# Kernel tuning notes

Measured on AMD Instinct MI355X. Metric: run time of the kernel, lower is better.

The kernel has to match this reference:

```python
import jax, jax.numpy as jnp
import numpy as np

B, L, E = 256, 4096, 64   # batch, seq_len, d_token
D = 128                   # d_model
H, DH = 4, 16             # attn heads, head dim
SH = 256                  # synapse_hidden
M = 8                     # memory_len
NED = 16                  # neuron_embed_dim
NH = 64                   # nlm_hidden
T = 8                     # n_ticks


def setup_inputs() -> dict:
    key = jax.random.key(0)
    ks = jax.random.split(key, 24)
    rn = lambda k, shape, fan: jax.random.normal(k, shape, jnp.float32) / np.sqrt(fan)
    return {
        "tokens": jax.random.normal(ks[0], (B, L, E), jnp.float32),
        "z0": jnp.zeros((D,), jnp.float32),
        "a0": jnp.zeros((D, M), jnp.float32),
        "ln_g": jnp.ones((D,), jnp.float32),
        "ln_b": jnp.zeros((D,), jnp.float32),
        "Wq": rn(ks[1], (E, D), D), "bq": jnp.zeros((E,), jnp.float32),
        "Wiq": rn(ks[2], (E, E), E), "biq": jnp.zeros((E,), jnp.float32),
        "Wik": rn(ks[3], (E, E), E), "bik": jnp.zeros((E,), jnp.float32),
        "Wiv": rn(ks[4], (E, E), E), "biv": jnp.zeros((E,), jnp.float32),
        "Wo": rn(ks[5], (E, E), E), "bo": jnp.zeros((E,), jnp.float32),
        "Ws1": rn(ks[6], (2 * SH, D + E), D + E), "bs1": jnp.zeros((2 * SH,), jnp.float32),
        "Ws2": rn(ks[7], (D, SH), SH), "bs2": jnp.zeros((D,), jnp.float32),
        "Wn1": rn(ks[8], (NH, M + NED), M + NED), "bn1": jnp.zeros((NH,), jnp.float32),
        "Wn2": rn(ks[9], (1, NH), NH), "bn2": jnp.zeros((1,), jnp.float32),
        "emb": jax.random.normal(ks[10], (D, NED), jnp.float32),
    }


def reference(tokens, z0, a0, ln_g, ln_b, Wq, bq, Wiq, biq, Wik, bik, Wiv, biv,
              Wo, bo, Ws1, bs1, Ws2, bs2, Wn1, bn1, Wn2, bn2, emb):
    b = tokens.shape[0]
    # K/V projections are tick-invariant -> compute once. (B,L,H,DH)
    k = (tokens @ Wik.T + bik).reshape(b, L, H, DH)
    v = (tokens @ Wiv.T + biv).reshape(b, L, H, DH)
    scale = 1.0 / np.sqrt(DH)

    def tick(carry, _):
        z, ah = carry  # z: (B,D), ah: (B,D,M)
        # query head: LayerNorm + Linear(D->E)
        mu = jnp.mean(z, -1, keepdims=True)
        var = jnp.mean((z - mu) ** 2, -1, keepdims=True)
        zn = (z - mu) * jax.lax.rsqrt(var + 1e-5) * ln_g + ln_b
        q = zn @ Wq.T + bq                               # (B,E)
        qh = (q @ Wiq.T + biq).reshape(b, H, DH)         # (B,H,DH)
        # single-query cross-attention
        scores = jnp.einsum("bhd,blhd->bhl", qh, k) * scale
        attw = jax.nn.softmax(scores, axis=-1)
        o = jnp.einsum("bhl,blhd->bhd", attw, v).reshape(b, E)
        o = o @ Wo.T + bo                                # (B,E)
        # synapse GLU-MLP
        s = jnp.concatenate([z, o], axis=-1) @ Ws1.T + bs1
        g1, g2 = jnp.split(s, 2, axis=-1)
        a = (g1 * jax.nn.sigmoid(g2)) @ Ws2.T + bs2      # (B,D)
        # roll history
        ah = jnp.concatenate([ah[:, :, 1:], a[:, :, None]], axis=-1)
        # per-neuron shared NLM with neuron embedding
        inp = jnp.concatenate([ah, jnp.broadcast_to(emb, (b, D, NED))], axis=-1)
        h = jax.nn.silu(inp @ Wn1.T + bn1)               # (B,D,NH)
        z_next = (h @ Wn2.T + bn2)[..., 0]               # (B,D)
        z = jnp.tanh(z_next)
        return (z, ah), z

    z = jnp.broadcast_to(z0, (b, D))
    ah = jnp.broadcast_to(a0, (b, D, M))
    _, zs = jax.lax.scan(tick, (z, ah), None, length=T)  # (T,B,D)
    return jnp.transpose(zs, (1, 0, 2))                  # (B,T,D)
```

## Files before the change

### kernel.cpp

```cpp
#include <hip/hip_runtime.h>

#define B_   256
#define L_   4096
#define E_   64
#define D_   128
#define H_   4
#define DH_  16
#define SH_  256
#define M_   8
#define NED_ 16
#define NH_  64
#define T_   8

typedef __attribute__((ext_vector_type(8))) short short8;
typedef __attribute__((ext_vector_type(4))) float f32x4;
typedef __attribute__((ext_vector_type(4))) unsigned int uint4v;
typedef __attribute__((ext_vector_type(2))) unsigned int uint2v;

#if defined(__has_builtin)
#if __has_builtin(__builtin_amdgcn_sdot4)
#define HAS_SDOT 1
#endif
#endif
#ifndef HAS_SDOT
#define HAS_SDOT 0
#endif

__device__ __forceinline__ float bf2f(unsigned short u) {
  union { unsigned int i; float f; } v; v.i = ((unsigned int)u) << 16; return v.f;
}
__device__ __forceinline__ unsigned short f2bf(float f) {
  union { float f; unsigned int i; } v; v.f = f;
  unsigned int x = v.i;
  return (unsigned short)((x + 0x7fffu + ((x >> 16) & 1u)) >> 16);
}
__device__ __forceinline__ float bflo(unsigned int u){ union { unsigned int i; float f; } v; v.i = u << 16;          return v.f; }
__device__ __forceinline__ float bfhi(unsigned int u){ union { unsigned int i; float f; } v; v.i = u & 0xffff0000u;  return v.f; }
__device__ __forceinline__ unsigned int pk2(float a, float b){
  return (unsigned int)f2bf(a) | ((unsigned int)f2bf(b) << 16);
}
__device__ __forceinline__ unsigned int pk4i(f32x4 x, float r) {
  const int a0 = (int)rintf(x[0] * r);
  const int a1 = (int)rintf(x[1] * r);
  const int a2 = (int)rintf(x[2] * r);
  const int a3 = (int)rintf(x[3] * r);
  return (unsigned int)(a0 & 255) | ((unsigned int)(a1 & 255) << 8) |
         ((unsigned int)(a2 & 255) << 16) | ((unsigned int)(a3 & 255) << 24);
}

template<int MODE>
__device__ __forceinline__ bool mode_ok(const void* ln_g) {
  const unsigned int w = ((const unsigned int*)ln_g)[0];
  return (w == 0x3F800000u) ? (MODE == 0) : (MODE == 1);
}
template<int MODE>
__device__ __forceinline__ float ldw(const void* p, long i) {
  if (MODE) return bf2f(((const unsigned short*)p)[i]);
  return ((const float*)p)[i];
}
template<int MODE>
__device__ __forceinline__ void stw(void* p, long i, float v) {
  if (MODE) ((unsigned short*)p)[i] = f2bf(v);
  else      ((float*)p)[i] = v;
}
template<int MODE>
__device__ __forceinline__ f32x4 ld4(const void* p, long off) {
  f32x4 r;
  if (MODE) {
    const uint2v u = *(const uint2v*)((const unsigned short*)p + off);
    r[0] = bflo(u[0]); r[1] = bfhi(u[0]); r[2] = bflo(u[1]); r[3] = bfhi(u[1]);
  } else {
    r = *(const f32x4*)((const float*)p + off);
  }
  return r;
}
template<int MODE>
__device__ __forceinline__ short8 ld8(const void* p, long off) {
  short8 r;
  if (MODE) {
    r = *(const short8*)((const unsigned short*)p + off);
  } else {
    const float* f = (const float*)p + off;
    const f32x4 f0 = *(const f32x4*)f;
    const f32x4 f1 = *(const f32x4*)(f + 4);
#pragma unroll
    for (int i = 0; i < 4; ++i) {
      r[i]     = (short)f2bf(f0[i]);
      r[4 + i] = (short)f2bf(f1[i]);
    }
  }
  return r;
}

template<int MODE>
__global__ void prep_kernel(const void* __restrict__ ln_g,
                            const void* __restrict__ Wik, const void* __restrict__ Wiv,
                            const void* __restrict__ Ws1, const void* __restrict__ Ws2,
                            unsigned short* __restrict__ Wbf,
                            float* __restrict__ Ws1T, float* __restrict__ Ws2T)
{
  if (!mode_ok<MODE>(ln_g)) return;
  const int idx = blockIdx.x * 256 + threadIdx.x;
  if (idx < 8192) {
    const float v = (idx < 4096) ? ldw<MODE>(Wik, idx) : ldw<MODE>(Wiv, idx - 4096);
    Wbf[idx] = f2bf(v);
  } else if (idx < 8192 + 98304) {
    const int j = idx - 8192;
    const int i = j >> 9, u = j & 511;
    Ws1T[j] = ldw<MODE>(Ws1, (long)u * 192 + i);
  } else if (idx < 8192 + 98304 + 32768) {
    const int j = idx - 8192 - 98304;
    const int i = j >> 7, u = j & 127;
    Ws2T[j] = ldw<MODE>(Ws2, (long)u * 256 + i);
  }
}

template<int MODE>
__global__ __launch_bounds__(256) void kv_proj_kernel(
    const void* __restrict__ ln_g,
    const void* __restrict__ tokens,
    const void* __restrict__ bik, const void* __restrict__ biv,
    const unsigned short* __restrict__ Wbf,
    unsigned char* __restrict__ K8, unsigned char* __restrict__ V8,
    unsigned int* __restrict__ SCb)
{
  if (!mode_ok<MODE>(ln_g)) return;
  const int lane = threadIdx.x & 63;
  const int wv   = threadIdx.x >> 6;
  const int m = lane & 15, quad = lane >> 4;
  const long row0 = (long)blockIdx.x * 128 + wv * 32;

  short8 tb[2][2];
#pragma unroll
  for (int nt = 0; nt < 2; ++nt) {
    const long ar = (row0 + nt * 16 + m) * 64;
    tb[nt][0] = ld8<MODE>(tokens, ar + quad * 8);
    tb[nt][1] = ld8<MODE>(tokens, ar + 32 + quad * 8);
  }

  f32x4 acc[8][2];
#pragma unroll
  for (int mt = 0; mt < 8; ++mt) { acc[mt][0] = 0.f; acc[mt][1] = 0.f; }

#pragma unroll
  for (int kt = 0; kt < 2; ++kt) {
    short8 wa[8];
#pragma unroll
    for (int mt = 0; mt < 8; ++mt)
      wa[mt] = *(const short8*)(Wbf + (mt * 16 + m) * 64 + kt * 32 + quad * 8);
#pragma unroll
    for (int mt = 0; mt < 8; ++mt) {
      acc[mt][0] = __builtin_amdgcn_mfma_f32_16x16x32_bf16(wa[mt], tb[0][kt], acc[mt][0], 0, 0, 0);
      acc[mt][1] = __builtin_amdgcn_mfma_f32_16x16x32_bf16(wa[mt], tb[1][kt], acc[mt][1], 0, 0, 0);
    }
  }

  const long b  = row0 >> 12;
  const int  l0 = (int)(row0 & 4095);
#pragma unroll
  for (int h = 0; h < 4; ++h) {
    const f32x4 bk = ld4<MODE>(bik, h * 16 + quad * 4);
    const f32x4 bv = ld4<MODE>(biv, h * 16 + quad * 4);
    const long rowbase = (b * H_ + h) * (long)L_ + l0;
#pragma unroll
    for (int nt = 0; nt < 2; ++nt) {
      const f32x4 xk = acc[h][nt] + bk;
      const f32x4 xv = acc[h + 4][nt] + bv;
      float ak = fmaxf(fmaxf(fabsf(xk[0]), fabsf(xk[1])), fmaxf(fabsf(xk[2]), fabsf(xk[3])));
      float av = fmaxf(fmaxf(fabsf(xv[0]), fabsf(xv[1])), fmaxf(fabsf(xv[2]), fabsf(xv[3])));
      ak = fmaxf(ak, __shfl_xor(ak, 16)); ak = fmaxf(ak, __shfl_xor(ak, 32));
      av = fmaxf(av, __shfl_xor(av, 16)); av = fmaxf(av, __shfl_xor(av, 32));
      const float rk = ak > 0.f ? 127.f / ak : 0.f;
      const float rv = av > 0.f ? 127.f / av : 0.f;
      const unsigned int uk = pk4i(xk, rk);
      const unsigned int uv = pk4i(xv, rv);
      const long row = rowbase + nt * 16 + m;
      ((unsigned int*)(K8 + row * 16))[quad] = uk;
      ((unsigned int*)(V8 + row * 16))[quad] = uv;
      if (quad == 0)
        SCb[row] = pk2(ak * (1.f / 127.f), av * (1.f / 127.f));
    }
  }
}

template<int MODE>
__global__ __launch_bounds__(1024, 4) void mega_kernel(
    const unsigned char* __restrict__ K8, const unsigned char* __restrict__ V8,
    const unsigned int* __restrict__ SCb,
    const float* __restrict__ Ws1T, const float* __restrict__ Ws2T,
    const void* __restrict__ z0, const void* __restrict__ a0,
    const void* __restrict__ ln_g, const void* __restrict__ ln_b,
    const void* __restrict__ Wq,  const void* __restrict__ bq,
    const void* __restrict__ Wiq, const void* __restrict__ biq,
    const void* __restrict__ Wo,  const void* __restrict__ bo,
    const void* __restrict__ bs1, const void* __restrict__ bs2,
    const void* __restrict__ Wn1, const void* __restrict__ bn1,
    const void* __restrict__ Wn2, const void* __restrict__ bn2,
    const void* __restrict__ emb,
    void* __restrict__ out)
{
  if (!mode_ok<MODE>(ln_g)) return;
  const int b = blockIdx.x, tid = threadIdx.x;
  const int lane = tid & 63, w = tid >> 6;

  __shared__ __align__(16) float z_l[128];
  __shared__ __align__(16) float ah_l[128][8];
  __shared__ __align__(16) float qh_l[64];
  __shared__ __align__(16) unsigned int qi_l[4][4];
  __shared__ float qsc_l[4];
  __shared__ __align__(16) float zo_l[192];
  __shared__ __align__(16) float s_l[512];
  __shared__ __align__(16) float spart[2][512];
  __shared__ __align__(16) float glu_l[256];
  __shared__ __align__(16) float al_l[128];
  __shared__ __align__(16) float p8[8][128];
  __shared__ float part[16][17];
  __shared__ __align__(16) float oat[64];
  __shared__ __align__(16) float znl[128];
  __shared__ __align__(16) float ql[64];
  __shared__ float red[16];

  if (tid < 128) {
    z_l[tid] = ldw<MODE>(z0, tid);
#pragma unroll
    for (int mm = 0; mm < 8; ++mm) ah_l[tid][mm] = ldw<MODE>(a0, tid * 8 + mm);
  }
  __syncthreads();

  for (int phase = 0; phase <= T_; ++phase) {
    if (phase > 0) {
      const int t = phase - 1;
      const int h = tid >> 8, r = tid & 255;
      const unsigned char* kp = K8 + ((long)(b * H_ + h) * L_) * 16;
      const unsigned char* vp = V8 + ((long)(b * H_ + h) * L_) * 16;
      const unsigned int*  scp = SCb + (long)(b * H_ + h) * L_;
#if HAS_SDOT
      const int qi0 = (int)qi_l[h][0], qi1 = (int)qi_l[h][1];
      const int qi2 = (int)qi_l[h][2], qi3 = (int)qi_l[h][3];
      const float qsch = qsc_l[h];
#else
      float q[16];
#pragma unroll
      for (int j = 0; j < 16; ++j) q[j] = qh_l[h * 16 + j] * 0.25f;
#endif
      float ssum = 0.f;
      float o[16];
#pragma unroll
      for (int j = 0; j < 16; ++j) o[j] = 0.f;

#pragma unroll 4
      for (int it = 0; it < 16; ++it) {
        const int l = r + it * 256;
        const uint4v kk = *(const uint4v*)(kp + (long)l * 16);
        const uint4v vv = *(const uint4v*)(vp + (long)l * 16);
        const unsigned int s = scp[l];
#if HAS_SDOT
        int id = 0;
        id = __builtin_amdgcn_sdot4((int)kk[0], qi0, id, false);
        id = __builtin_amdgcn_sdot4((int)kk[1], qi1, id, false);
        id = __builtin_amdgcn_sdot4((int)kk[2], qi2, id, false);
        id = __builtin_amdgcn_sdot4((int)kk[3], qi3, id, false);
        const float sc = (float)id * bflo(s) * qsch;
#else
        float scf = 0.f;
#pragma unroll
        for (int d = 0; d < 4; ++d) {
          const unsigned int u = kk[d];
          scf = fmaf(q[d * 4 + 0], (float)((int)(u << 24) >> 24), scf);
          scf = fmaf(q[d * 4 + 1], (float)((int)(u << 16) >> 24), scf);
          scf = fmaf(q[d * 4 + 2], (float)((int)(u <<  8) >> 24), scf);
          scf = fmaf(q[d * 4 + 3], (float)((int)u >> 24),          scf);
        }
        const float sc = scf * bflo(s);
#endif
        const float pw = __expf(sc);
        ssum += pw;
        const float pv = pw * bfhi(s);
#pragma unroll
        for (int d = 0; d < 4; ++d) {
          const unsigned int u = vv[d];
          o[d * 4 + 0] = fmaf(pv, (float)((int)(u << 24) >> 24), o[d * 4 + 0]);
          o[d * 4 + 1] = fmaf(pv, (float)((int)(u << 16) >> 24), o[d * 4 + 1]);
          o[d * 4 + 2] = fmaf(pv, (float)((int)(u <<  8) >> 24), o[d * 4 + 2]);
          o[d * 4 + 3] = fmaf(pv, (float)((int)u >> 24),          o[d * 4 + 3]);
        }
      }
#pragma unroll
      for (int off = 1; off < 64; off <<= 1) {
        ssum += __shfl_xor(ssum, off);
#pragma unroll
        for (int j = 0; j < 16; ++j) o[j] += __shfl_xor(o[j], off);
      }
      if (lane == 0) {
        part[w][16] = ssum;
#pragma unroll
        for (int j = 0; j < 16; ++j) part[w][j] = o[j];
      }
      __syncthreads();
      if (tid < 128) zo_l[tid] = z_l[tid];
      if (tid < 64) {
        const int hh = tid >> 4, j = tid & 15;
        const float O = part[hh * 4][j] + part[hh * 4 + 1][j] +
                        part[hh * 4 + 2][j] + part[hh * 4 + 3][j];
        const float S = part[hh * 4][16] + part[hh * 4 + 1][16] +
                        part[hh * 4 + 2][16] + part[hh * 4 + 3][16];
        oat[tid] = O / S;
      }
      __syncthreads();
      if (tid < 64) {
        f32x4 av = 0.f;
        const long wr = (long)tid * 64;
#pragma unroll
        for (int i = 0; i < 16; ++i)
          av += (*(const f32x4*)&oat[i * 4]) * ld4<MODE>(Wo, wr + i * 4);
        zo_l[128 + tid] = av[0] + av[1] + av[2] + av[3] + ldw<MODE>(bo, tid);
      }
      __syncthreads();
      {
        const int u = tid & 511, p = tid >> 9;
        float a = 0.f;
#pragma unroll 8
        for (int i = 0; i < 96; ++i)
          a = fmaf(zo_l[p * 96 + i], Ws1T[(p * 96 + i) * 512 + u], a);
        spart[p][u] = a;
      }
      __syncthreads();
      if (tid < 512) s_l[tid] = spart[0][tid] + spart[1][tid] + ldw<MODE>(bs1, tid);
      __syncthreads();
      if (tid < 256)
        glu_l[tid] = s_l[tid] * (1.f / (1.f + __expf(-s_l[tid + 256])));
      __syncthreads();
      {
        const int u = tid & 127, p = tid >> 7;
        float a = 0.f;
#pragma unroll 8
        for (int i = 0; i < 32; ++i)
          a = fmaf(glu_l[p * 32 + i], Ws2T[(p * 32 + i) * 128 + u], a);
        p8[p][u] = a;
      }
      __syncthreads();
      if (tid < 128) {
        float a = ldw<MODE>(bs2, tid);
#pragma unroll
        for (int k = 0; k < 8; ++k) a += p8[k][tid];
        al_l[tid] = a;
      }
      __syncthreads();
      {
        const int d = tid >> 3, p = tid & 7;
        float ahv[8];
#pragma unroll
        for (int c = 0; c < 7; ++c) ahv[c] = ah_l[d][c + 1];
        ahv[7] = al_l[d];
        f32x4 ev[4];
#pragma unroll
        for (int c = 0; c < 4; ++c) ev[c] = ld4<MODE>(emb, d * 16 + c * 4);
        float pr = 0.f;
#pragma unroll
        for (int uu = 0; uu < 8; ++uu) {
          const int u = p * 8 + uu;
          const long wr = (long)u * 24;
          f32x4 av = ld4<MODE>(Wn1, wr) * (*(const f32x4*)&ahv[0])
                   + ld4<MODE>(Wn1, wr + 4) * (*(const f32x4*)&ahv[4]);
#pragma unroll
          for (int c = 0; c < 4; ++c) av += ev[c] * ld4<MODE>(Wn1, wr + 8 + c * 4);
          const float acc = av[0] + av[1] + av[2] + av[3] + ldw<MODE>(bn1, u);
          const float hs = acc * (1.f / (1.f + __expf(-acc)));
          pr = fmaf(hs, ldw<MODE>(Wn2, u), pr);
        }
        pr += __shfl_xor(pr, 1);
        pr += __shfl_xor(pr, 2);
        pr += __shfl_xor(pr, 4);
        const float znew = tanhf(pr + ldw<MODE>(bn2, 0));
        __syncthreads();
        if (p == 0) {
#pragma unroll
          for (int c = 0; c < 8; ++c) ah_l[d][c] = ahv[c];
          z_l[d] = znew;
          stw<MODE>(out, ((long)b * T_ + t) * D_ + d, znew);
        }
      }
      __syncthreads();
      if (t == T_ - 1) break;
    }
    if (tid < 128) {
      const float x = z_l[tid];
      float sx = x, sxx = x * x;
#pragma unroll
      for (int off = 1; off < 64; off <<= 1) {
        sx  += __shfl_xor(sx, off);
        sxx += __shfl_xor(sxx, off);
      }
      if (lane == 0) { red[w] = sx; red[8 + w] = sxx; }
    }
    __syncthreads();
    {
      const float mu  = (red[0] + red[1]) * (1.f / 128.f);
      const float ex2 = (red[8] + red[9]) * (1.f / 128.f);
      const float rstd = rsqrtf(ex2 - mu * mu + 1e-5f);
      if (tid < 128)
        znl[tid] = (z_l[tid] - mu) * rstd * ldw<MODE>(ln_g, tid) + ldw<MODE>(ln_b, tid);
    }
    __syncthreads();
    if (tid < 64) {
      f32x4 av = 0.f;
      const long wr = (long)tid * 128;
#pragma unroll
      for (int i = 0; i < 32; ++i)
        av += (*(const f32x4*)&znl[i * 4]) * ld4<MODE>(Wq, wr + i * 4);
      ql[tid] = av[0] + av[1] + av[2] + av[3] + ldw<MODE>(bq, tid);
    }
    __syncthreads();
    if (tid < 64) {
      f32x4 av = 0.f;
      const long wr = (long)tid * 64;
#pragma unroll
      for (int i = 0; i < 16; ++i)
        av += (*(const f32x4*)&ql[i * 4]) * ld4<MODE>(Wiq, wr + i * 4);
      qh_l[tid] = av[0] + av[1] + av[2] + av[3] + ldw<MODE>(biq, tid);
    }
    __syncthreads();
    if (tid < 4) {
      float am = 0.f;
#pragma unroll
      for (int j = 0; j < 16; ++j) am = fmaxf(am, fabsf(qh_l[tid * 16 + j]));
      const float rq = am > 0.f ? 127.f / am : 0.f;
      qsc_l[tid] = am * (0.25f / 127.f);
#pragma unroll
      for (int dd = 0; dd < 4; ++dd) {
        const int a0 = (int)rintf(qh_l[tid * 16 + dd * 4 + 0] * rq);
        const int a1 = (int)rintf(qh_l[tid * 16 + dd * 4 + 1] * rq);
        const int a2 = (int)rintf(qh_l[tid * 16 + dd * 4 + 2] * rq);
        const int a3 = (int)rintf(qh_l[tid * 16 + dd * 4 + 3] * rq);
        qi_l[tid][dd] = (unsigned int)(a0 & 255) | ((unsigned int)(a1 & 255) << 8) |
                        ((unsigned int)(a2 & 255) << 16) | ((unsigned int)(a3 & 255) << 24);
      }
    }
    __syncthreads();
  }
}

extern "C" void kernel_launch(void* const* d_in, const int* in_sizes, int n_in,
                              void* d_out, int out_size, void* d_ws, size_t ws_size,
                              hipStream_t stream)
{
  const void* tokens = d_in[0];
  const void* z0   = d_in[1];
  const void* a0   = d_in[2];
  const void* ln_g = d_in[3];
  const void* ln_b = d_in[4];
  const void* Wq   = d_in[5];
  const void* bq   = d_in[6];
  const void* Wiq  = d_in[7];
  const void* biq  = d_in[8];
  const void* Wik  = d_in[9];
  const void* bik  = d_in[10];
  const void* Wiv  = d_in[11];
  const void* biv  = d_in[12];
  const void* Wo   = d_in[13];
  const void* bo   = d_in[14];
  const void* Ws1  = d_in[15];
  const void* bs1  = d_in[16];
  const void* Ws2  = d_in[17];
  const void* bs2  = d_in[18];
  const void* Wn1  = d_in[19];
  const void* bn1  = d_in[20];
  const void* Wn2  = d_in[21];
  const void* bn2  = d_in[22];
  const void* emb  = d_in[23];

  const long K8_B = (long)B_ * H_ * L_ * 16;
  const long SC_B = (long)B_ * H_ * L_ * 4;
  char* ws = (char*)d_ws;
  const long offW = 2 * K8_B + SC_B;
  if (ws_size < (size_t)(offW + 16384 + 393216 + 131072)) return;
  unsigned char* K8  = (unsigned char*)(ws);
  unsigned char* V8  = (unsigned char*)(ws + K8_B);
  unsigned int*  SCb = (unsigned int*)(ws + 2 * K8_B);
  unsigned short* Wbf = (unsigned short*)(ws + offW);
  float* Ws1T = (float*)(ws + offW + 16384);
  float* Ws2T = (float*)(ws + offW + 16384 + 393216);

  prep_kernel<0><<<544, 256, 0, stream>>>(ln_g, Wik, Wiv, Ws1, Ws2, Wbf, Ws1T, Ws2T);
  prep_kernel<1><<<544, 256, 0, stream>>>(ln_g, Wik, Wiv, Ws1, Ws2, Wbf, Ws1T, Ws2T);

  kv_proj_kernel<0><<<(B_ * L_) / 128, 256, 0, stream>>>(ln_g, tokens, bik, biv, Wbf, K8, V8, SCb);
  kv_proj_kernel<1><<<(B_ * L_) / 128, 256, 0, stream>>>(ln_g, tokens, bik, biv, Wbf, K8, V8, SCb);

  mega_kernel<0><<<B_, 1024, 0, stream>>>(K8, V8, SCb, Ws1T, Ws2T, z0, a0, ln_g, ln_b,
      Wq, bq, Wiq, biq, Wo, bo, bs1, bs2, Wn1, bn1, Wn2, bn2, emb, d_out);
  mega_kernel<1><<<B_, 1024, 0, stream>>>(K8, V8, SCb, Ws1T, Ws2T, z0, a0, ln_g, ln_b,
      Wq, bq, Wiq, biq, Wo, bo, bs1, bs2, Wn1, bn1, Wn2, bn2, emb, d_out);
}
```

Before: 956.3 us.

## Stage K/V int8 rows into LDS via async global_load_lds with 4-deep pipeline

The attention inner loop now loads K, V and scale rows with global_load_lds into a per-wave 4-slot LDS ring, prefetching three iterations ahead and gating each consume on explicit vmcnt waits. V is stored as offset-binary uint8 so it can be decoded with cheap zero-extends, and the +128 bias is removed at the end with a single fma against the accumulated weight sum. The separate reduction buffers are merged into one scratch array so the large staging buffer fits in LDS. The intent is to hide global-load latency and cut decode ALU work, at the cost of about 147KB of LDS per block, which limits occupancy, plus fragile hand-written waitcnt accounting.

```diff
diff --git a/kernel.cpp b/kernel.cpp
--- a/kernel.cpp
+++ b/kernel.cpp
@@ -12,6 +12,9 @@
 #define NH_  64
 #define T_   8
 
+#define AS1 __attribute__((address_space(1)))
+#define AS3 __attribute__((address_space(3)))
+
 typedef __attribute__((ext_vector_type(8))) short short8;
 typedef __attribute__((ext_vector_type(4))) float f32x4;
 typedef __attribute__((ext_vector_type(4))) unsigned int uint4v;
@@ -44,6 +47,14 @@
   const int a1 = (int)rintf(x[1] * r);
   const int a2 = (int)rintf(x[2] * r);
   const int a3 = (int)rintf(x[3] * r);
+  return (unsigned int)(a0 & 255) | ((unsigned int)(a1 & 255) << 8) |
+         ((unsigned int)(a2 & 255) << 16) | ((unsigned int)(a3 & 255) << 24);
+}
+__device__ __forceinline__ unsigned int pk4u(f32x4 x, float r) {
+  const int a0 = (int)rintf(x[0] * r) + 128;
+  const int a1 = (int)rintf(x[1] * r) + 128;
+  const int a2 = (int)rintf(x[2] * r) + 128;
+  const int a3 = (int)rintf(x[3] * r) + 128;
   return (unsigned int)(a0 & 255) | ((unsigned int)(a1 & 255) << 8) |
          ((unsigned int)(a2 & 255) << 16) | ((unsigned int)(a3 & 255) << 24);
 }
@@ -173,7 +184,7 @@
       const float rk = ak > 0.f ? 127.f / ak : 0.f;
       const float rv = av > 0.f ? 127.f / av : 0.f;
       const unsigned int uk = pk4i(xk, rk);
-      const unsigned int uv = pk4i(xv, rv);
+      const unsigned int uv = pk4u(xv, rv);
       const long row = rowbase + nt * 16 + m;
       ((unsigned int*)(K8 + row * 16))[quad] = uk;
       ((unsigned int*)(V8 + row * 16))[quad] = uv;
@@ -203,6 +214,8 @@
   const int b = blockIdx.x, tid = threadIdx.x;
   const int lane = tid & 63, w = tid >> 6;
 
+  __shared__ __align__(16) char stageb[16 * 4 * 2304];
+  __shared__ __align__(16) float scratch[1024];
   __shared__ __align__(16) float z_l[128];
   __shared__ __align__(16) float ah_l[128][8];
   __shared__ __align__(16) float qh_l[64];
@@ -210,11 +223,8 @@
   __shared__ float qsc_l[4];
   __shared__ __align__(16) float zo_l[192];
   __shared__ __align__(16) float s_l[512];
-  __shared__ __align__(16) float spart[2][512];
   __shared__ __align__(16) float glu_l[256];
   __shared__ __align__(16) float al_l[128];
-  __shared__ __align__(16) float p8[8][128];
-  __shared__ float part[16][17];
   __shared__ __align__(16) float oat[64];
   __shared__ __align__(16) float znl[128];
   __shared__ __align__(16) float ql[64];
@@ -227,13 +237,30 @@
   }
   __syncthreads();
 
+  const int h = w >> 2;
+  const long headrow = ((long)(b * H_) + h) * L_;
+  const char* kp8 = (const char*)K8 + headrow * 16;
+  const char* vp8 = (const char*)V8 + headrow * 16;
+  const char* sp8 = (const char*)SCb + headrow * 4;
+  AS3 char* stg_w = (AS3 char*)stageb + w * (4 * 2304);
+
+#define STAGE(IT) do {                                                          \
+    const long ro_ = (long)((w & 3) * 64) + (long)(IT) * 256;                   \
+    AS3 char* dst_ = stg_w + ((IT) & 3) * 2304;                                 \
+    __builtin_amdgcn_global_load_lds(                                           \
+        (const AS1 unsigned int*)(kp8 + ro_ * 16 + lane * 16),                  \
+        (AS3 unsigned int*)(dst_), 16, 0, 0);                                   \
+    __builtin_amdgcn_global_load_lds(                                           \
+        (const AS1 unsigned int*)(vp8 + ro_ * 16 + lane * 16),                  \
+        (AS3 unsigned int*)(dst_ + 1024), 16, 0, 0);                            \
+    __builtin_amdgcn_global_load_lds(                                           \
+        (const AS1 unsigned int*)(sp8 + ro_ * 4 + lane * 4),                    \
+        (AS3 unsigned int*)(dst_ + 2048), 4, 0, 0);                             \
+  } while (0)
+
   for (int phase = 0; phase <= T_; ++phase) {
     if (phase > 0) {
       const int t = phase - 1;
-      const int h = tid >> 8, r = tid & 255;
-      const unsigned char* kp = K8 + ((long)(b * H_ + h) * L_) * 16;
-      const unsigned char* vp = V8 + ((long)(b * H_ + h) * L_) * 16;
-      const unsigned int*  scp = SCb + (long)(b * H_ + h) * L_;
 #if HAS_SDOT
       const int qi0 = (int)qi_l[h][0], qi1 = (int)qi_l[h][1];
       const int qi2 = (int)qi_l[h][2], qi3 = (int)qi_l[h][3];
@@ -243,48 +270,67 @@
 #pragma unroll
       for (int j = 0; j < 16; ++j) q[j] = qh_l[h * 16 + j] * 0.25f;
 #endif
-      float ssum = 0.f;
+      float ssum = 0.f, spv = 0.f;
       float o[16];
 #pragma unroll
       for (int j = 0; j < 16; ++j) o[j] = 0.f;
 
-#pragma unroll 4
-      for (int it = 0; it < 16; ++it) {
-        const int l = r + it * 256;
-        const uint4v kk = *(const uint4v*)(kp + (long)l * 16);
-        const uint4v vv = *(const uint4v*)(vp + (long)l * 16);
-        const unsigned int s = scp[l];
+      STAGE(0); STAGE(1); STAGE(2);
+
 #if HAS_SDOT
-        int id = 0;
-        id = __builtin_amdgcn_sdot4((int)kk[0], qi0, id, false);
-        id = __builtin_amdgcn_sdot4((int)kk[1], qi1, id, false);
-        id = __builtin_amdgcn_sdot4((int)kk[2], qi2, id, false);
-        id = __builtin_amdgcn_sdot4((int)kk[3], qi3, id, false);
+#define SCORE(kk)                                                              \
+        int id = 0;                                                            \
+        id = __builtin_amdgcn_sdot4((int)kk[0], qi0, id, false);               \
+        id = __builtin_amdgcn_sdot4((int)kk[1], qi1, id, false);               \
+        id = __builtin_amdgcn_sdot4((int)kk[2], qi2, id, false);               \
+        id = __builtin_amdgcn_sdot4((int)kk[3], qi3, id, false);               \
         const float sc = (float)id * bflo(s) * qsch;
 #else
-        float scf = 0.f;
-#pragma unroll
-        for (int d = 0; d < 4; ++d) {
-          const unsigned int u = kk[d];
-          scf = fmaf(q[d * 4 + 0], (float)((int)(u << 24) >> 24), scf);
-          scf = fmaf(q[d * 4 + 1], (float)((int)(u << 16) >> 24), scf);
-          scf = fmaf(q[d * 4 + 2], (float)((int)(u <<  8) >> 24), scf);
-          scf = fmaf(q[d * 4 + 3], (float)((int)u >> 24),          scf);
-        }
+#define SCORE(kk)                                                              \
+        float scf = 0.f;                                                       \
+        _Pragma("unroll")                                                      \
+        for (int d_ = 0; d_ < 4; ++d_) {                                       \
+          const unsigned int u_ = kk[d_];                                      \
+          scf = fmaf(q[d_ * 4 + 0], (float)((int)(u_ << 24) >> 24), scf);      \
+          scf = fmaf(q[d_ * 4 + 1], (float)((int)(u_ << 16) >> 24), scf);      \
+          scf = fmaf(q[d_ * 4 + 2], (float)((int)(u_ <<  8) >> 24), scf);      \
+          scf = fmaf(q[d_ * 4 + 3], (float)((int)u_ >> 24),          scf);     \
+        }                                                                      \
         const float sc = scf * bflo(s);
 #endif
-        const float pw = __expf(sc);
-        ssum += pw;
-        const float pv = pw * bfhi(s);
-#pragma unroll
-        for (int d = 0; d < 4; ++d) {
-          const unsigned int u = vv[d];
-          o[d * 4 + 0] = fmaf(pv, (float)((int)(u << 24) >> 24), o[d * 4 + 0]);
-          o[d * 4 + 1] = fmaf(pv, (float)((int)(u << 16) >> 24), o[d * 4 + 1]);
-          o[d * 4 + 2] = fmaf(pv, (float)((int)(u <<  8) >> 24), o[d * 4 + 2]);
-          o[d * 4 + 3] = fmaf(pv, (float)((int)u >> 24),          o[d * 4 + 3]);
-        }
-      }
+
+#define ITER(IT, VM) do {                                                      \
+        asm volatile("s_waitcnt vmcnt(" #VM ")" ::: "memory");                 \
+        const AS3 char* slot_ = (const AS3 char*)stg_w + ((IT) & 3) * 2304;    \
+        const uint4v kk = *(const AS3 uint4v*)(slot_ + lane * 16);             \
+        const uint4v vv = *(const AS3 uint4v*)(slot_ + 1024 + lane * 16);      \
+        const unsigned int s = *(const AS3 unsigned int*)(slot_ + 2048 + lane * 4); \
+        asm volatile("s_waitcnt lgkmcnt(3)" ::: "memory");                     \
+        if ((IT) + 3 < 16) STAGE((IT) + 3);                                    \
+        SCORE(kk)                                                              \
+        const float pw = __expf(sc);                                           \
+        ssum += pw;                                                            \
+        const float pv = pw * bfhi(s);                                         \
+        spv += pv;                                                             \
+        _Pragma("unroll")                                                      \
+        for (int d_ = 0; d_ < 4; ++d_) {                                       \
+          const unsigned int u_ = vv[d_];                                      \
+          o[d_ * 4 + 0] = fmaf(pv, (float)(unsigned char)(u_),       o[d_ * 4 + 0]); \
+          o[d_ * 4 + 1] = fmaf(pv, (float)(unsigned char)(u_ >> 8),  o[d_ * 4 + 1]); \
+          o[d_ * 4 + 2] = fmaf(pv, (float)(unsigned char)(u_ >> 16), o[d_ * 4 + 2]); \
+          o[d_ * 4 + 3] = fmaf(pv, (float)(unsigned char)(u_ >> 24), o[d_ * 4 + 3]); \
+        }                                                                      \
+      } while (0)
+
+      ITER(0, 6);  ITER(1, 6);  ITER(2, 6);  ITER(3, 6);
+      ITER(4, 6);  ITER(5, 6);  ITER(6, 6);  ITER(7, 6);
+      ITER(8, 6);  ITER(9, 6);  ITER(10, 6); ITER(11, 6);
+      ITER(12, 6); ITER(13, 6); ITER(14, 3); ITER(15, 0);
+#undef ITER
+#undef SCORE
+
+#pragma unroll
+      for (int j = 0; j < 16; ++j) o[j] = fmaf(-128.f, spv, o[j]);
 #pragma unroll
       for (int off = 1; off < 64; off <<= 1) {
         ssum += __shfl_xor(ssum, off);
@@ -292,18 +338,18 @@
         for (int j = 0; j < 16; ++j) o[j] += __shfl_xor(o[j], off);
       }
       if (lane == 0) {
-        part[w][16] = ssum;
-#pragma unroll
-        for (int j = 0; j < 16; ++j) part[w][j] = o[j];
+        scratch[w * 17 + 16] = ssum;
+#pragma unroll
+        for (int j = 0; j < 16; ++j) scratch[w * 17 + j] = o[j];
       }
       __syncthreads();
       if (tid < 128) zo_l[tid] = z_l[tid];
       if (tid < 64) {
         const int hh = tid >> 4, j = tid & 15;
-        const float O = part[hh * 4][j] + part[hh * 4 + 1][j] +
-                        part[hh * 4 + 2][j] + part[hh * 4 + 3][j];
-        const float S = part[hh * 4][16] + part[hh * 4 + 1][16] +
-                        part[hh * 4 + 2][16] + part[hh * 4 + 3][16];
+        const float O = scratch[(hh * 4) * 17 + j] + scratch[(hh * 4 + 1) * 17 + j] +
+                        scratch[(hh * 4 + 2) * 17 + j] + scratch[(hh * 4 + 3) * 17 + j];
+        const float S = scratch[(hh * 4) * 17 + 16] + scratch[(hh * 4 + 1) * 17 + 16] +
+                        scratch[(hh * 4 + 2) * 17 + 16] + scratch[(hh * 4 + 3) * 17 + 16];
         oat[tid] = O / S;
       }
       __syncthreads();
@@ -322,10 +368,10 @@
 #pragma unroll 8
         for (int i = 0; i < 96; ++i)
           a = fmaf(zo_l[p * 96 + i], Ws1T[(p * 96 + i) * 512 + u], a);
-        spart[p][u] = a;
-      }
-      __syncthreads();
-      if (tid < 512) s_l[tid] = spart[0][tid] + spart[1][tid] + ldw<MODE>(bs1, tid);
+        scratch[p * 512 + u] = a;
+      }
+      __syncthreads();
+      if (tid < 512) s_l[tid] = scratch[tid] + scratch[512 + tid] + ldw<MODE>(bs1, tid);
       __syncthreads();
       if (tid < 256)
         glu_l[tid] = s_l[tid] * (1.f / (1.f + __expf(-s_l[tid + 256])));
@@ -336,13 +382,13 @@
 #pragma unroll 8
         for (int i = 0; i < 32; ++i)
           a = fmaf(glu_l[p * 32 + i], Ws2T[(p * 32 + i) * 128 + u], a);
-        p8[p][u] = a;
+        scratch[p * 128 + u] = a;
       }
       __syncthreads();
       if (tid < 128) {
         float a = ldw<MODE>(bs2, tid);
 #pragma unroll
-        for (int k = 0; k < 8; ++k) a += p8[k][tid];
+        for (int k = 0; k < 8; ++k) a += scratch[k * 128 + tid];
         al_l[tid] = a;
       }
       __syncthreads();
@@ -438,6 +484,7 @@
     }
     __syncthreads();
   }
+#undef STAGE
 }
 
 extern "C" void kernel_launch(void* const* d_in, const int* in_sizes, int n_in,
```

After: 1.442 ms. 50.8% more time.
